# Optimization experiments

Hardware: AMD Instinct MI355X
Metric: run time of the kernel (lower is better)

The kernel has to match this reference:

```python
import jax, jax.numpy as jnp
import numpy as np

TOP_K = 8
NUM_EXPERTS = 64
ALPHA = 1e-3  # aux_loss_alpha


def setup_inputs() -> dict:
    key = jax.random.key(0)
    k1, k2 = jax.random.split(key)
    B, S, D, E = 4, 4096, 2048, NUM_EXPERTS
    hidden_states = jax.random.normal(k1, (B, S, D), dtype=jnp.float32)
    # kaiming_uniform_(a=sqrt(5)) on an (E, D) matrix -> U(-1/sqrt(D), 1/sqrt(D))
    bound = 1.0 / np.sqrt(D)
    weight = jax.random.uniform(k2, (E, D), dtype=jnp.float32, minval=-bound, maxval=bound)
    return {"hidden_states": hidden_states, "weight": weight}


def reference(hidden_states, weight):
    B, S, D = hidden_states.shape
    E = weight.shape[0]
    x = hidden_states.reshape(-1, D)                      # [B*S, D]
    logits = jnp.einsum('td,ed->te', x, weight)           # [B*S, E]
    scores = jax.nn.softmax(logits, axis=-1)
    topk_weight, topk_idx = jax.lax.top_k(scores, TOP_K)  # [B*S, K]
    # norm_topk_prob (top_k > 1)
    topk_weight = topk_weight / (topk_weight.sum(axis=-1, keepdims=True) + 1e-20)
    # training-mode seq_aux auxiliary loss
    idx_per_seq = topk_idx.reshape(B, S * TOP_K)          # [B, S*K]
    ce = jax.vmap(lambda idx: jnp.zeros((E,), scores.dtype).at[idx].add(1.0))(idx_per_seq)
    ce = ce / (S * TOP_K / E)                             # [B, E]
    seq_scores_mean = scores.reshape(B, S, E).mean(axis=1)  # [B, E]
    aux_loss = (ce * seq_scores_mean).sum(axis=1).mean() * ALPHA
    return topk_idx, topk_weight, aux_loss
```

## Files before the change

### kernel.cpp

```cpp
#include <hip/hip_runtime.h>
#include <math.h>

#define TT 16384
#define DD 2048
#define EE 64
#define KTOP 8
#define BM 64
#define BK 32
#define NT (DD / BK)
#define SL 4096
#define BB 4
#define XSTR 68

__device__ __forceinline__ float np_expf(float x) {
    const float LOG2E = 1.442695040888963407359924681001892137f;
    const float MAGIC = 0x1.800000p+23f;
    const float C1 = -6.93145752e-1f;
    const float C2 = -1.42860677e-6f;
    float q = __fmul_rn(x, LOG2E);
    q = __fadd_rn(q, MAGIC);
    q = __fsub_rn(q, MAGIC);
    x = __fmaf_rn(q, C1, x);
    x = __fmaf_rn(q, C2, x);
    float num = __fmaf_rn(5.082762527590693718096e-04f, x, 6.757896990527504603057e-03f);
    num = __fmaf_rn(num, x, 5.114512081637298353406e-02f);
    num = __fmaf_rn(num, x, 2.473615434895520810817e-01f);
    num = __fmaf_rn(num, x, 7.257664613233124478488e-01f);
    num = __fmaf_rn(num, x, 9.999999999980870924916e-01f);
    float den = __fmaf_rn(2.159509375685829852307e-02f, x, -2.742335390411667452936e-01f);
    den = __fmaf_rn(den, x, 1.0f);
    const float quot = __fdiv_rn(num, den);
    const int qi = (int)q;
    const float sc = __uint_as_float((unsigned int)(127 + qi) << 23);
    return __fmul_rn(quot, sc);
}

__device__ __forceinline__ bool is_fold(int kt1) {
    return kt1 == 10 || kt1 == 20 || kt1 == 30 || kt1 == 40 ||
           kt1 == 50 || kt1 == 57 || kt1 == 64;
}

__global__ __launch_bounds__(256) void moe_gate_main(
    const float* __restrict__ X, const float* __restrict__ W,
    float* __restrict__ out, float* __restrict__ ws_cnt, float* __restrict__ ws_ssum)
{
    __shared__ float Xs[2][BK * XSTR];
    __shared__ float Wsh[2][BK * XSTR];
    __shared__ float Ls[BM * XSTR];
    __shared__ float cnt[EE];

    const int tid  = threadIdx.x;
    const int row0 = blockIdx.x * BM;
    const int tr   = tid >> 4;
    const int tc   = tid & 15;

    float tot[4][4];
    float ch[2][4][4];
#pragma unroll
    for (int i = 0; i < 4; ++i)
#pragma unroll
        for (int j = 0; j < 4; ++j) {
            tot[i][j] = 0.f; ch[0][i][j] = 0.f; ch[1][i][j] = 0.f;
        }

    if (tid < EE) cnt[tid] = 0.f;

    float xr[8], wr[8];
#pragma unroll
    for (int j = 0; j < 8; ++j) {
        const int el = j * 256 + tid;
        const int r = el >> 5, kk = el & 31;
        xr[j] = X[(size_t)(row0 + r) * DD + kk];
        wr[j] = W[(size_t)r * DD + kk];
    }
#pragma unroll
    for (int j = 0; j < 8; ++j) {
        const int el = j * 256 + tid;
        const int r = el >> 5, kk = el & 31;
        Xs[0][kk * XSTR + r]  = xr[j];
        Wsh[0][kk * XSTR + r] = wr[j];
    }

    for (int kt = 0; kt < NT; ++kt) {
        __syncthreads();
        const int cur = kt & 1;
        if (kt + 1 < NT) {
            const int kbase = (kt + 1) * BK;
#pragma unroll
            for (int j = 0; j < 8; ++j) {
                const int el = j * 256 + tid;
                const int r = el >> 5, kk = el & 31;
                xr[j] = X[(size_t)(row0 + r) * DD + kbase + kk];
                wr[j] = W[(size_t)r * DD + kbase + kk];
            }
        }
#pragma unroll
        for (int kk = 0; kk < BK; ++kk) {
            const int p = (kk >> 2) & 1;
            const float4 a = *(const float4*)&Xs[cur][kk * XSTR + 4 * tr];
            const float4 b = *(const float4*)&Wsh[cur][kk * XSTR + 4 * tc];
            ch[p][0][0] = __fmaf_rn(a.x, b.x, ch[p][0][0]);
            ch[p][0][1] = __fmaf_rn(a.x, b.y, ch[p][0][1]);
            ch[p][0][2] = __fmaf_rn(a.x, b.z, ch[p][0][2]);
            ch[p][0][3] = __fmaf_rn(a.x, b.w, ch[p][0][3]);
            ch[p][1][0] = __fmaf_rn(a.y, b.x, ch[p][1][0]);
            ch[p][1][1] = __fmaf_rn(a.y, b.y, ch[p][1][1]);
            ch[p][1][2] = __fmaf_rn(a.y, b.z, ch[p][1][2]);
            ch[p][1][3] = __fmaf_rn(a.y, b.w, ch[p][1][3]);
            ch[p][2][0] = __fmaf_rn(a.z, b.x, ch[p][2][0]);
            ch[p][2][1] = __fmaf_rn(a.z, b.y, ch[p][2][1]);
            ch[p][2][2] = __fmaf_rn(a.z, b.z, ch[p][2][2]);
            ch[p][2][3] = __fmaf_rn(a.z, b.w, ch[p][2][3]);
            ch[p][3][0] = __fmaf_rn(a.w, b.x, ch[p][3][0]);
            ch[p][3][1] = __fmaf_rn(a.w, b.y, ch[p][3][1]);
            ch[p][3][2] = __fmaf_rn(a.w, b.z, ch[p][3][2]);
            ch[p][3][3] = __fmaf_rn(a.w, b.w, ch[p][3][3]);
        }
        if (is_fold(kt + 1)) {
#pragma unroll
            for (int i = 0; i < 4; ++i)
#pragma unroll
                for (int j = 0; j < 4; ++j) {
                    const float c2 = __fadd_rn(ch[0][i][j], ch[1][i][j]);
                    tot[i][j] = __fadd_rn(tot[i][j], c2);
                    ch[0][i][j] = 0.f; ch[1][i][j] = 0.f;
                }
        }
        if (kt + 1 < NT) {
#pragma unroll
            for (int j = 0; j < 8; ++j) {
                const int el = j * 256 + tid;
                const int r = el >> 5, kk = el & 31;
                Xs[cur ^ 1][kk * XSTR + r]  = xr[j];
                Wsh[cur ^ 1][kk * XSTR + r] = wr[j];
            }
        }
    }

#pragma unroll
    for (int i = 0; i < 4; ++i) {
        float4 v; v.x = tot[i][0]; v.y = tot[i][1]; v.z = tot[i][2]; v.w = tot[i][3];
        *(float4*)&Ls[(4 * tr + i) * XSTR + 4 * tc] = v;
    }
    __syncthreads();

    if (tid < BM) {
        const int r = tid;
        float l[EE];
#pragma unroll
        for (int q = 0; q < 16; ++q) {
            const float4 v = *(const float4*)&Ls[r * XSTR + 4 * q];
            l[4 * q] = v.x; l[4 * q + 1] = v.y; l[4 * q + 2] = v.z; l[4 * q + 3] = v.w;
        }
        float m = l[0];
#pragma unroll
        for (int e = 1; e < EE; ++e) m = fmaxf(m, l[e]);

        float u[EE];
#pragma unroll
        for (int e = 0; e < EE; ++e) u[e] = np_expf(__fsub_rn(l[e], m));

        float rr[8];
#pragma unroll
        for (int j = 0; j < 8; ++j) rr[j] = u[j];
#pragma unroll
        for (int c = 1; c < 8; ++c)
#pragma unroll
            for (int j = 0; j < 8; ++j) rr[j] = __fadd_rn(rr[j], u[8 * c + j]);
        const float z = __fadd_rn(
            __fadd_rn(__fadd_rn(rr[0], rr[1]), __fadd_rn(rr[2], rr[3])),
            __fadd_rn(__fadd_rn(rr[4], rr[5]), __fadd_rn(rr[6], rr[7])));

        float s[EE];
#pragma unroll
        for (int e = 0; e < EE; ++e) s[e] = __fdiv_rn(u[e], z);

        float pv = 3.4e38f; int pi = -1;
        float wk[KTOP]; int ti[KTOP]; float wsum = 0.f;
#pragma unroll
        for (int k = 0; k < KTOP; ++k) {
            float best = -3.4e38f; int bi = 0;
#pragma unroll
            for (int e = 0; e < EE; ++e) {
                const bool elig   = (s[e] < pv) || ((s[e] == pv) && (e > pi));
                const bool better = elig && (s[e] > best);
                best = better ? s[e] : best;
                bi   = better ? e    : bi;
            }
            wk[k] = best; ti[k] = bi; wsum = __fadd_rn(wsum, best);
            pv = best; pi = bi;
        }
        const float den = __fadd_rn(wsum, 1e-20f);

        const size_t t = (size_t)row0 + r;
        float4 o0, o1;
        o0.x = (float)ti[0]; o0.y = (float)ti[1]; o0.z = (float)ti[2]; o0.w = (float)ti[3];
        o1.x = (float)ti[4]; o1.y = (float)ti[5]; o1.z = (float)ti[6]; o1.w = (float)ti[7];
        *(float4*)&out[t * 8]     = o0;
        *(float4*)&out[t * 8 + 4] = o1;
        float* outw = out + (size_t)TT * KTOP;
        o0.x = __fdiv_rn(wk[0], den); o0.y = __fdiv_rn(wk[1], den);
        o0.z = __fdiv_rn(wk[2], den); o0.w = __fdiv_rn(wk[3], den);
        o1.x = __fdiv_rn(wk[4], den); o1.y = __fdiv_rn(wk[5], den);
        o1.z = __fdiv_rn(wk[6], den); o1.w = __fdiv_rn(wk[7], den);
        *(float4*)&outw[t * 8]     = o0;
        *(float4*)&outw[t * 8 + 4] = o1;

#pragma unroll
        for (int k = 0; k < KTOP; ++k) atomicAdd(&cnt[ti[k]], 1.f);

#pragma unroll
        for (int q = 0; q < 16; ++q) {
            float4 v;
            v.x = s[4 * q]; v.y = s[4 * q + 1]; v.z = s[4 * q + 2]; v.w = s[4 * q + 3];
            *(float4*)&Ls[r * XSTR + 4 * q] = v;
        }
    }
    __syncthreads();

    if (tid < EE) {
        const int e = tid;
        float cs = 0.f;
#pragma unroll
        for (int r2 = 0; r2 < BM; ++r2) cs += Ls[r2 * XSTR + e];
        const int b = row0 / SL;
        atomicAdd(&ws_ssum[b * EE + e], cs);
        atomicAdd(&ws_cnt[b * EE + e], cnt[e]);
    }
}

__global__ void moe_gate_aux(const float* __restrict__ ws_cnt,
                             const float* __restrict__ ws_ssum,
                             float* __restrict__ out_aux)
{
    __shared__ float red[4];
    const int tid = threadIdx.x;
    float v = ws_cnt[tid] * ws_ssum[tid];
#pragma unroll
    for (int m = 32; m; m >>= 1) v += __shfl_xor(v, m, 64);
    if ((tid & 63) == 0) red[tid >> 6] = v;
    __syncthreads();
    if (tid == 0) {
        const float tot = red[0] + red[1] + red[2] + red[3];
        out_aux[0] = tot * (1e-3f / ((float)BB * 512.f * (float)SL));
    }
}

extern "C" void kernel_launch(void* const* d_in, const int* in_sizes, int n_in,
                              void* d_out, int out_size, void* d_ws, size_t ws_size,
                              hipStream_t stream)
{
    const float* X = (const float*)d_in[0];
    const float* W = (const float*)d_in[1];
    float* out  = (float*)d_out;
    float* cnt  = (float*)d_ws;
    float* ssum = cnt + BB * EE;
    hipMemsetAsync(d_ws, 0, 2 * BB * EE * sizeof(float), stream);
    moe_gate_main<<<TT / BM, 256, 0, stream>>>(X, W, out, cnt, ssum);
    moe_gate_aux<<<1, 256, 0, stream>>>(cnt, ssum, out + (size_t)2 * TT * KTOP);
}
```

Measured before the change: 236.2 us.

## Halve row tile to 32, alias staging and epilogue LDS, precompute load pointers

```diff
diff --git a/kernel.cpp b/kernel.cpp
--- a/kernel.cpp
+++ b/kernel.cpp
@@ -5,12 +5,14 @@
 #define DD 2048
 #define EE 64
 #define KTOP 8
-#define BM 64
+#define BM 32
 #define BK 32
 #define NT (DD / BK)
 #define SL 4096
 #define BB 4
-#define XSTR 68
+#define XS_STR 36
+#define WS_STR 68
+#define LS_STR 68
 
 __device__ __forceinline__ float np_expf(float x) {
     const float LOG2E = 1.442695040888963407359924681001892137f;
@@ -44,9 +46,10 @@
     const float* __restrict__ X, const float* __restrict__ W,
     float* __restrict__ out, float* __restrict__ ws_cnt, float* __restrict__ ws_ssum)
 {
-    __shared__ float Xs[2][BK * XSTR];
-    __shared__ float Wsh[2][BK * XSTR];
-    __shared__ float Ls[BM * XSTR];
+    __shared__ union {
+        struct { float Xs[2][BK * XS_STR]; float Wsh[2][BK * WS_STR]; } st;
+        struct { float L[BM * LS_STR]; } ep;
+    } sh;
     __shared__ float cnt[EE];
 
     const int tid  = threadIdx.x;
@@ -54,10 +57,10 @@
     const int tr   = tid >> 4;
     const int tc   = tid & 15;
 
-    float tot[4][4];
-    float ch[2][4][4];
-#pragma unroll
-    for (int i = 0; i < 4; ++i)
+    float tot[2][4];
+    float ch[2][2][4];
+#pragma unroll
+    for (int i = 0; i < 2; ++i)
 #pragma unroll
         for (int j = 0; j < 4; ++j) {
             tot[i][j] = 0.f; ch[0][i][j] = 0.f; ch[1][i][j] = 0.f;
@@ -65,40 +68,47 @@
 
     if (tid < EE) cnt[tid] = 0.f;
 
-    float xr[8], wr[8];
+    const float* xptr[4]; int xdst[4];
+#pragma unroll
+    for (int j = 0; j < 4; ++j) {
+        const int el = j * 256 + tid;
+        const int r = el >> 5, kk = el & 31;
+        xptr[j] = X + (size_t)(row0 + r) * DD + kk;
+        xdst[j] = kk * XS_STR + r;
+    }
+    const float* wptr[8]; int wdst[8];
 #pragma unroll
     for (int j = 0; j < 8; ++j) {
         const int el = j * 256 + tid;
         const int r = el >> 5, kk = el & 31;
-        xr[j] = X[(size_t)(row0 + r) * DD + kk];
-        wr[j] = W[(size_t)r * DD + kk];
-    }
-#pragma unroll
-    for (int j = 0; j < 8; ++j) {
-        const int el = j * 256 + tid;
-        const int r = el >> 5, kk = el & 31;
-        Xs[0][kk * XSTR + r]  = xr[j];
-        Wsh[0][kk * XSTR + r] = wr[j];
-    }
+        wptr[j] = W + (size_t)r * DD + kk;
+        wdst[j] = kk * WS_STR + r;
+    }
+
+    float xr[4], wr[8];
+#pragma unroll
+    for (int j = 0; j < 4; ++j) { xr[j] = *xptr[j]; xptr[j] += BK; }
+#pragma unroll
+    for (int j = 0; j < 8; ++j) { wr[j] = *wptr[j]; wptr[j] += BK; }
+#pragma unroll
+    for (int j = 0; j < 4; ++j) sh.st.Xs[0][xdst[j]] = xr[j];
+#pragma unroll
+    for (int j = 0; j < 8; ++j) sh.st.Wsh[0][wdst[j]] = wr[j];
 
     for (int kt = 0; kt < NT; ++kt) {
         __syncthreads();
         const int cur = kt & 1;
         if (kt + 1 < NT) {
-            const int kbase = (kt + 1) * BK;
-#pragma unroll
-            for (int j = 0; j < 8; ++j) {
-                const int el = j * 256 + tid;
-                const int r = el >> 5, kk = el & 31;
-                xr[j] = X[(size_t)(row0 + r) * DD + kbase + kk];
-                wr[j] = W[(size_t)r * DD + kbase + kk];
-            }
+#pragma unroll
+            for (int j = 0; j < 4; ++j) { xr[j] = *xptr[j]; xptr[j] += BK; }
+#pragma unroll
+            for (int j = 0; j < 8; ++j) { wr[j] = *wptr[j]; wptr[j] += BK; }
         }
 #pragma unroll
         for (int kk = 0; kk < BK; ++kk) {
             const int p = (kk >> 2) & 1;
-            const float4 a = *(const float4*)&Xs[cur][kk * XSTR + 4 * tr];
-            const float4 b = *(const float4*)&Wsh[cur][kk * XSTR + 4 * tc];
+            const float2 a = *(const float2*)&sh.st.Xs[cur][kk * XS_STR + 2 * tr];
+            const float4 b = *(const float4*)&sh.st.Wsh[cur][kk * WS_STR + 4 * tc];
             ch[p][0][0] = __fmaf_rn(a.x, b.x, ch[p][0][0]);
             ch[p][0][1] = __fmaf_rn(a.x, b.y, ch[p][0][1]);
             ch[p][0][2] = __fmaf_rn(a.x, b.z, ch[p][0][2]);
@@ -107,18 +117,10 @@
             ch[p][1][1] = __fmaf_rn(a.y, b.y, ch[p][1][1]);
             ch[p][1][2] = __fmaf_rn(a.y, b.z, ch[p][1][2]);
             ch[p][1][3] = __fmaf_rn(a.y, b.w, ch[p][1][3]);
-            ch[p][2][0] = __fmaf_rn(a.z, b.x, ch[p][2][0]);
-            ch[p][2][1] = __fmaf_rn(a.z, b.y, ch[p][2][1]);
-            ch[p][2][2] = __fmaf_rn(a.z, b.z, ch[p][2][2]);
-            ch[p][2][3] = __fmaf_rn(a.z, b.w, ch[p][2][3]);
-            ch[p][3][0] = __fmaf_rn(a.w, b.x, ch[p][3][0]);
-            ch[p][3][1] = __fmaf_rn(a.w, b.y, ch[p][3][1]);
-            ch[p][3][2] = __fmaf_rn(a.w, b.z, ch[p][3][2]);
-            ch[p][3][3] = __fmaf_rn(a.w, b.w, ch[p][3][3]);
         }
         if (is_fold(kt + 1)) {
 #pragma unroll
-            for (int i = 0; i < 4; ++i)
+            for (int i = 0; i < 2; ++i)
 #pragma unroll
                 for (int j = 0; j < 4; ++j) {
                     const float c2 = __fadd_rn(ch[0][i][j], ch[1][i][j]);
@@ -128,19 +130,17 @@
         }
         if (kt + 1 < NT) {
 #pragma unroll
-            for (int j = 0; j < 8; ++j) {
-                const int el = j * 256 + tid;
-                const int r = el >> 5, kk = el & 31;
-                Xs[cur ^ 1][kk * XSTR + r]  = xr[j];
-                Wsh[cur ^ 1][kk * XSTR + r] = wr[j];
-            }
-        }
-    }
-
-#pragma unroll
-    for (int i = 0; i < 4; ++i) {
+            for (int j = 0; j < 4; ++j) sh.st.Xs[cur ^ 1][xdst[j]] = xr[j];
+#pragma unroll
+            for (int j = 0; j < 8; ++j) sh.st.Wsh[cur ^ 1][wdst[j]] = wr[j];
+        }
+    }
+
+    __syncthreads();
+#pragma unroll
+    for (int i = 0; i < 2; ++i) {
         float4 v; v.x = tot[i][0]; v.y = tot[i][1]; v.z = tot[i][2]; v.w = tot[i][3];
-        *(float4*)&Ls[(4 * tr + i) * XSTR + 4 * tc] = v;
+        *(float4*)&sh.ep.L[(2 * tr + i) * LS_STR + 4 * tc] = v;
     }
     __syncthreads();
 
@@ -149,7 +149,7 @@
         float l[EE];
 #pragma unroll
         for (int q = 0; q < 16; ++q) {
-            const float4 v = *(const float4*)&Ls[r * XSTR + 4 * q];
+            const float4 v = *(const float4*)&sh.ep.L[r * LS_STR + 4 * q];
             l[4 * q] = v.x; l[4 * q + 1] = v.y; l[4 * q + 2] = v.z; l[4 * q + 3] = v.w;
         }
         float m = l[0];
@@ -213,7 +213,7 @@
         for (int q = 0; q < 16; ++q) {
             float4 v;
             v.x = s[4 * q]; v.y = s[4 * q + 1]; v.z = s[4 * q + 2]; v.w = s[4 * q + 3];
-            *(float4*)&Ls[r * XSTR + 4 * q] = v;
+            *(float4*)&sh.ep.L[r * LS_STR + 4 * q] = v;
         }
     }
     __syncthreads();
@@ -222,7 +222,7 @@
         const int e = tid;
         float cs = 0.f;
 #pragma unroll
-        for (int r2 = 0; r2 < BM; ++r2) cs += Ls[r2 * XSTR + e];
+        for (int r2 = 0; r2 < BM; ++r2) cs += sh.ep.L[r2 * LS_STR + e];
         const int b = row0 / SL;
         atomicAdd(&ws_ssum[b * EE + e], cs);
         atomicAdd(&ws_cnt[b * EE + e], cnt[e]);
```

After: 478.6 us. 2.03x slower.
